# Kernel optimization log

Hardware: AMD Instinct MI355X
Metric: run time of the kernel (lower is better)

The kernel has to match this reference:

```python
import jax, jax.numpy as jnp
import numpy as np
import math

B, N, DIM, H, DH, NNULL = 2, 2048, 1024, 16, 64, 2
SCALE = 8.0
LN_EPS = 1e-5


def _alibi_slopes(heads):
    # heads is a power of 2 here (16): slopes = start * start**i
    start = 2.0 ** (-(2.0 ** (-(math.log2(heads) - 3))))
    return np.array([start * (start ** i) for i in range(heads)], dtype=np.float32)


def setup_inputs() -> dict:
    key = jax.random.key(0)
    ks = jax.random.split(key, 6)
    inner = H * DH
    return {
        "x": jax.random.normal(ks[0], (B, N, DIM), dtype=jnp.float32),
        "norm_g": jnp.ones((DIM,), jnp.float32),
        "norm_b": jnp.zeros((DIM,), jnp.float32),
        "Wq": jax.random.normal(ks[1], (DIM, inner), jnp.float32) * 0.02,
        "Wkv": jax.random.normal(ks[2], (DIM, 2 * inner), jnp.float32) * 0.02,
        "q_scale": jnp.ones((DH,), jnp.float32),
        "k_scale": jnp.ones((DH,), jnp.float32),
        "null_kv": jax.random.normal(ks[3], (H, 2 * NNULL, DH), jnp.float32),
        "Wout": jax.random.normal(ks[4], (inner, DIM), jnp.float32) * 0.02,
    }


def _l2norm(t):
    # matches F.normalize: x / max(||x||, 1e-12)
    n = jnp.sqrt(jnp.sum(t * t, axis=-1, keepdims=True))
    return t / jnp.maximum(n, 1e-12)


def reference(x, norm_g, norm_b, Wq, Wkv, q_scale, k_scale, null_kv, Wout):
    b, n, dim = x.shape
    h, dh, nn = H, DH, NNULL
    j = n + nn

    # NOTE: faithful to source -- K/V come from the PRE-norm x (kv_input bound
    # before x = self.norm(x)); only Q uses the LayerNorm'd x.
    mu = jnp.mean(x, axis=-1, keepdims=True)
    var = jnp.mean((x - mu) ** 2, axis=-1, keepdims=True)
    xn = (x - mu) * jax.lax.rsqrt(var + LN_EPS) * norm_g + norm_b

    q = (xn @ Wq).reshape(b, n, h, dh).transpose(0, 2, 1, 3)          # b h n d
    kv = x @ Wkv
    k, v = jnp.split(kv, 2, axis=-1)
    k = k.reshape(b, n, h, dh).transpose(0, 2, 1, 3)                   # b h n d
    v = v.reshape(b, n, h, dh).transpose(0, 2, 1, 3)

    # null kv: (h, 2*nn, dh) -> (h, nn, 2, dh)
    null = null_kv.reshape(h, nn, 2, dh)
    nk = jnp.broadcast_to(null[:, :, 0, :][None], (b, h, nn, dh))
    nv = jnp.broadcast_to(null[:, :, 1, :][None], (b, h, nn, dh))
    k = jnp.concatenate([nk, k], axis=2)                               # b h j d
    v = jnp.concatenate([nv, v], axis=2)

    q = _l2norm(q) * q_scale
    k = _l2norm(k) * k_scale

    sim = jnp.einsum('bhid,bhjd->bhij', q, k) * SCALE                  # b h n j

    # ALiBi bias: rows at positions j-n..j-1, cols 0..j-1
    irow = jnp.arange(j - n, j)
    jcol = jnp.arange(j)
    bias = -jnp.abs(jcol[None, :] - irow[:, None]).astype(sim.dtype)   # (n, j)
    slopes = jnp.asarray(_alibi_slopes(h))[:, None, None]              # (h,1,1)
    sim = sim + slopes * bias

    # causal mask: triu with offset j - n + 1 (null kv always visible)
    causal = jnp.triu(jnp.ones((n, j), dtype=bool), k=j - n + 1)
    neg = jnp.finfo(sim.dtype).max
    sim = jnp.where(causal[None, None], -neg, sim)

    attn = jax.nn.softmax(sim, axis=-1)
    out = jnp.einsum('bhij,bhjd->bhid', attn, v)
    out = out.transpose(0, 2, 1, 3).reshape(b, n, h * dh)
    return out @ Wout
```

## Files before the change

kernel.cpp:

```cpp
#include <hip/hip_runtime.h>
#include <hip/hip_bf16.h>
#include <stdint.h>

#define H_    16
#define N_    2048
#define DIM_  1024
#define DH_   64
#define NN_   2
#define J_    2050
#define JP_   2112
#define B_    2
#define M_    4096
#define NSEG_ 84

#define S8L_  11.541560327111707f
#define LOG2E_ 1.4426950408889634f

typedef unsigned short u16;
typedef unsigned int u32;
typedef short bf16x8 __attribute__((ext_vector_type(8)));
typedef float f32x4 __attribute__((ext_vector_type(4)));

__device__ __forceinline__ u16 f2b(float f) {
  union { float f; unsigned int i; } v; v.f = f;
  unsigned int r = v.i + 0x7fffu + ((v.i >> 16) & 1u);
  return (u16)(r >> 16);
}
__device__ __forceinline__ float b2f(u16 u) {
  union { unsigned int i; float f; } v; v.i = ((unsigned int)u) << 16; return v.f;
}
__device__ __forceinline__ float lo2f(u32 u) {
  union { u32 i; float f; } v; v.i = u << 16; return v.f;
}
__device__ __forceinline__ float hi2f(u32 u) {
  union { u32 i; float f; } v; v.i = u & 0xffff0000u; return v.f;
}
__device__ __forceinline__ void unp8(const uint4 u, float* d) {
  d[0] = lo2f(u.x); d[1] = hi2f(u.x); d[2] = lo2f(u.y); d[3] = hi2f(u.y);
  d[4] = lo2f(u.z); d[5] = hi2f(u.z); d[6] = lo2f(u.w); d[7] = hi2f(u.w);
}
__device__ __forceinline__ u32 pk2(float a, float b) {
  union { __hip_bfloat162 h; u32 u; } x;
  x.h = __float22bfloat162_rn(make_float2(a, b));
  return x.u;
}
__device__ __forceinline__ void dma16(const u16* g, u16* l) {
  __builtin_amdgcn_global_load_lds(
      (const __attribute__((address_space(1))) u32*)(const void*)g,
      (__attribute__((address_space(3))) u32*)(void*)l, 16, 0, 0);
}

__global__ __launch_bounds__(256) void ktranspose_cast(const float* __restrict__ in,
                                                       u16* __restrict__ out, int R, int C) {
  __shared__ float tile[32][33];
  int tx = threadIdx.x & 31, ty = threadIdx.x >> 5;
  int c0 = blockIdx.x * 32, r0 = blockIdx.y * 32;
  #pragma unroll
  for (int i = 0; i < 32; i += 8)
    tile[ty + i][tx] = in[(size_t)(r0 + ty + i) * C + c0 + tx];
  __syncthreads();
  #pragma unroll
  for (int i = 0; i < 32; i += 8)
    out[(size_t)(c0 + ty + i) * R + r0 + tx] = f2b(tile[tx][ty + i]);
}

__global__ __launch_bounds__(256) void lnorm_k(const float* __restrict__ x,
                                               const float* __restrict__ g,
                                               const float* __restrict__ bb,
                                               u16* __restrict__ xn,
                                               u16* __restrict__ xbf) {
  int row = blockIdx.x;
  int t = threadIdx.x;
  float4 rw = *(const float4*)(x + (size_t)row * DIM_ + t * 4);
  float v0 = rw.x, v1 = rw.y, v2 = rw.z, v3 = rw.w;
  uint2 cw;
  cw.x = pk2(v0, v1);
  cw.y = pk2(v2, v3);
  *(uint2*)(xbf + (size_t)row * DIM_ + t * 4) = cw;
  float s = v0 + v1 + v2 + v3;
  float ss = v0 * v0 + v1 * v1 + v2 * v2 + v3 * v3;
  #pragma unroll
  for (int o = 32; o; o >>= 1) { s += __shfl_xor(s, o, 64); ss += __shfl_xor(ss, o, 64); }
  __shared__ float red[8];
  int lane = t & 63, w = t >> 6;
  if (lane == 0) { red[w] = s; red[4 + w] = ss; }
  __syncthreads();
  float S = red[0] + red[1] + red[2] + red[3];
  float SS = red[4] + red[5] + red[6] + red[7];
  float mu = S * (1.0f / DIM_);
  float var = SS * (1.0f / DIM_) - mu * mu;
  float rs = rsqrtf(var + 1e-5f);
  float4 gv = *(const float4*)(g + t * 4);
  float4 bv = *(const float4*)(bb + t * 4);
  uint2 ow;
  ow.x = pk2((v0 - mu) * rs * gv.x + bv.x, (v1 - mu) * rs * gv.y + bv.y);
  ow.y = pk2((v2 - mu) * rs * gv.z + bv.z, (v3 - mu) * rs * gv.w + bv.w);
  *(uint2*)(xn + (size_t)row * DIM_ + t * 4) = ow;
}

template <int MODE>
__global__ __launch_bounds__(256) void gemm_k(const u16* __restrict__ A,
                                              const u16* __restrict__ BT,
                                              void* __restrict__ dst0,
                                              void* __restrict__ dst1,
                                              const float* __restrict__ scale,
                                              int M, int Nc, int K) {
  __shared__ u16 As[128 * 64];
  __shared__ u16 Bs[64 * 64];
  int tid = threadIdx.x, wv = tid >> 6, lane = tid & 63;
  int fm = lane & 15, fg = lane >> 4;
  int row0 = blockIdx.y * 128, col0 = blockIdx.x * 64;
  f32x4 acc[2][4] = {};
  int srow = lane >> 3;
  int skb = ((lane & 7) ^ srow) * 8;
  const u16* Ag = A + (size_t)(row0 + wv * 32 + srow) * K + skb;
  const u16* Bg = BT + (size_t)(col0 + wv * 16 + srow) * K + skb;
  u16* AsW = As + (wv * 32) * 64;
  u16* BsW = Bs + (wv * 16) * 64;
  int fr7 = fm & 7;
  int ak0 = (fg ^ fr7) * 8;
  int ak1 = ((fg + 4) ^ fr7) * 8;
  for (int k0 = 0; k0 < K; k0 += 64) {
    __syncthreads();
    dma16(Ag + k0,                    AsW);
    dma16(Ag + (size_t)8 * K + k0,    AsW + 8 * 64);
    dma16(Ag + (size_t)16 * K + k0,   AsW + 16 * 64);
    dma16(Ag + (size_t)24 * K + k0,   AsW + 24 * 64);
    dma16(Bg + k0,                    BsW);
    dma16(Bg + (size_t)8 * K + k0,    BsW + 8 * 64);
    __syncthreads();
    bf16x8 af0[2], af1[2], bf0[4], bf1[4];
    #pragma unroll
    for (int mt = 0; mt < 2; mt++) {
      int rbase = (wv * 32 + mt * 16 + fm) * 64;
      af0[mt] = *(const bf16x8*)&As[rbase + ak0];
      af1[mt] = *(const bf16x8*)&As[rbase + ak1];
    }
    #pragma unroll
    for (int nt = 0; nt < 4; nt++) {
      int rbase = (nt * 16 + fm) * 64;
      bf0[nt] = *(const bf16x8*)&Bs[rbase + ak0];
      bf1[nt] = *(const bf16x8*)&Bs[rbase + ak1];
    }
    #pragma unroll
    for (int mt = 0; mt < 2; mt++)
      #pragma unroll
      for (int nt = 0; nt < 4; nt++) {
        acc[mt][nt] = __builtin_amdgcn_mfma_f32_16x16x32_bf16(af0[mt], bf0[nt], acc[mt][nt], 0, 0, 0);
        acc[mt][nt] = __builtin_amdgcn_mfma_f32_16x16x32_bf16(af1[mt], bf1[nt], acc[mt][nt], 0, 0, 0);
      }
  }
  if (MODE == 1) {
    float* C = (float*)dst0;
    #pragma unroll
    for (int mt = 0; mt < 2; mt++)
      #pragma unroll
      for (int r = 0; r < 4; r++) {
        int m = row0 + wv * 32 + mt * 16 + fg * 4 + r;
        #pragma unroll
        for (int nt = 0; nt < 4; nt++)
          C[(size_t)m * Nc + col0 + nt * 16 + fm] = acc[mt][nt][r];
      }
  } else {
    bool isK = (MODE == 2) || (col0 < 1024);
    int h = (isK ? col0 : col0 - 1024) >> 6;
    float sv[4];
    if (isK) {
      #pragma unroll
      for (int nt = 0; nt < 4; nt++) sv[nt] = scale[nt * 16 + fm];
      if (MODE == 2) {
        #pragma unroll
        for (int nt = 0; nt < 4; nt++) sv[nt] *= S8L_;
      }
    }
    u16* Do = (u16*)((MODE == 3 && !isK) ? dst1 : dst0);
    #pragma unroll
    for (int mt = 0; mt < 2; mt++) {
      #pragma unroll
      for (int r = 0; r < 4; r++) {
        float inv = 1.0f;
        if (isK) {
          float ssp = 0.0f;
          #pragma unroll
          for (int nt = 0; nt < 4; nt++) ssp += acc[mt][nt][r] * acc[mt][nt][r];
          #pragma unroll
          for (int o = 1; o <= 8; o <<= 1) ssp += __shfl_xor(ssp, o, 64);
          inv = 1.0f / fmaxf(sqrtf(ssp), 1e-12f);
        }
        int m = row0 + wv * 32 + mt * 16 + fg * 4 + r;
        int b = m >> 11, n = m & 2047;
        size_t base;
        if (MODE == 2)      base = (((size_t)(b * H_ + h)) * N_ + n) * 64;
        else if (isK)       base = (((size_t)(b * H_ + h)) * JP_ + (n + NN_)) * 64;
        else                base = (((size_t)(b * H_ + h)) * J_ + (n + NN_)) * 64;
        #pragma unroll
        for (int nt = 0; nt < 4; nt++) {
          float val = acc[mt][nt][r];
          if (isK) val = val * inv * sv[nt];
          Do[base + nt * 16 + fm] = f2b(val);
        }
      }
    }
  }
}

__global__ __launch_bounds__(256) void vtransp_k(const u16* __restrict__ Vb,
                                                 const float* __restrict__ nkv,
                                                 const float* __restrict__ ks,
                                                 u16* __restrict__ Kb,
                                                 u16* __restrict__ VTp) {
  __shared__ u16 tile[64][80];
  int t = threadIdx.x;
  int c = blockIdx.x, bh = blockIdx.y, h = bh & 15;
  int jl = t >> 2, dc = (t & 3) * 16;
  int j = c * 64 + jl;
  if (j < NN_) {
    float kvv[16];
    float kssp = 0.0f;
    #pragma unroll
    for (int e = 0; e < 16; e++) {
      float vv = nkv[(size_t)(h * 4 + 2 * j + 1) * 64 + dc + e];
      tile[jl][dc + e] = f2b(vv);
      float kv = nkv[(size_t)(h * 4 + 2 * j) * 64 + dc + e];
      kvv[e] = kv; kssp += kv * kv;
    }
    kssp += __shfl_xor(kssp, 1, 64);
    kssp += __shfl_xor(kssp, 2, 64);
    float inv = 1.0f / fmaxf(sqrtf(kssp), 1e-12f);
    #pragma unroll
    for (int e = 0; e < 16; e++)
      Kb[((size_t)bh * JP_ + j) * 64 + dc + e] = f2b(kvv[e] * inv * ks[dc + e]);
  } else if (j < J_) {
    const uint4* src = (const uint4*)(Vb + ((size_t)bh * J_ + j) * 64 + dc);
    *(uint4*)&tile[jl][dc] = src[0];
    *(uint4*)&tile[jl][dc + 8] = src[1];
  } else {
    uint4 z = {0, 0, 0, 0};
    *(uint4*)&tile[jl][dc] = z;
    *(uint4*)&tile[jl][dc + 8] = z;
  }
  __syncthreads();
  int d = t >> 2, p0 = (t & 3) * 16;
  u16 tmp[16] __attribute__((aligned(16)));
  #pragma unroll
  for (int e = 0; e < 16; e++) {
    int pos = p0 + e;
    int h2 = pos >> 5, rem = pos & 31;
    int fgp = rem >> 3, tt = rem & 7;
    int nt = tt >> 2, r = tt & 3;
    int jloc = (h2 * 2 + nt) * 16 + fgp * 4 + r;
    tmp[e] = tile[jloc][d];
  }
  uint4* dstp = (uint4*)(VTp + ((size_t)bh * 64 + d) * JP_ + c * 64 + p0);
  dstp[0] = ((uint4*)tmp)[0];
  dstp[1] = ((uint4*)tmp)[1];
}

__global__ __launch_bounds__(256, 6) void attn_k(const u16* __restrict__ Qn,
                                                 const u16* __restrict__ Kb,
                                                 const u16* __restrict__ VTp,
                                                 const float* __restrict__ qs,
                                                 const float* __restrict__ ks,
                                                 u16* __restrict__ partials) {
  __shared__ u16 Ks0[64 * 32], Ks1[64 * 32];
  __shared__ u16 Vs0[64 * 32], Vs1[64 * 32];
  int tid = threadIdx.x;
  int wv = tid >> 6, lane = tid & 63;
  int fm = lane & 15, fg = lane >> 4;
  int bh = blockIdx.y, h = bh & 15;
  int cum = 0, qt = 0, seg = 0;
  #pragma unroll 1
  for (int i = 0; i < 32; i++) {
    int t = 31 - i, s = (t + 9) >> 3;
    if ((int)blockIdx.x < cum + s) { qt = t; seg = (int)blockIdx.x - cum; break; }
    cum += s;
  }
  int q0 = qt * 64;
  int q = q0 + wv * 16 + fm;
  float slope = exp2f(-0.5f * (float)(h + 1));
  float prod = fabsf(qs[lane] * ks[lane]);
  #pragma unroll
  for (int o = 32; o; o >>= 1) prod = fmaxf(prod, __shfl_xor(prod, o, 64));
  float MbL = 8.0f * prod * LOG2E_;
  float slopeL = slope * LOG2E_;
  const u16* qp = Qn + ((size_t)bh * N_ + q) * 64 + fg * 8;
  bf16x8 qf0 = *(const bf16x8*)(qp);
  bf16x8 qf1 = *(const bf16x8*)(qp + 32);
  f32x4 accO[4] = {};
  float lp = 0.0f;
  int lr = lane >> 2;
  int kbs = ((lane & 3) ^ ((lane >> 3) & 3)) * 8;
  int fs = (fg ^ ((fm >> 1) & 3)) * 8;
  const u16* KbBH = Kb + (size_t)bh * JP_ * 64;
  const u16* VTbh = VTp + (size_t)bh * 64 * JP_;
  int c0 = seg * 8;
  int c1 = min(c0 + 8, qt + 2);
  float bias0 = slopeL * (float)(c0 * 64 + fg * 4 - q - 2) - MbL;
  float sr1 = slopeL, sr2 = slopeL * 2.0f, sr3 = slopeL * 3.0f;
  float s16 = slopeL * 16.0f;
  float d64 = slopeL * 64.0f;
  for (int c = c0; c < c1; c++) {
    int jb = c * 64;
    __syncthreads();
    const u16* Kg = KbBH + (size_t)(jb + wv * 16 + lr) * 64 + kbs;
    dma16(Kg,      Ks0 + wv * 512);
    dma16(Kg + 32, Ks1 + wv * 512);
    const u16* Vg = VTbh + (size_t)(wv * 16 + lr) * JP_ + jb + kbs;
    dma16(Vg,      Vs0 + wv * 512);
    dma16(Vg + 32, Vs1 + wv * 512);
    __syncthreads();
    f32x4 accS[4] = {};
    #pragma unroll
    for (int nt = 0; nt < 4; nt++) {
      bf16x8 kf0 = *(const bf16x8*)&Ks0[(nt * 16 + fm) * 32 + fs];
      accS[nt] = __builtin_amdgcn_mfma_f32_16x16x32_bf16(kf0, qf0, accS[nt], 0, 0, 0);
      bf16x8 kf1 = *(const bf16x8*)&Ks1[(nt * 16 + fm) * 32 + fs];
      accS[nt] = __builtin_amdgcn_mfma_f32_16x16x32_bf16(kf1, qf1, accS[nt], 0, 0, 0);
    }
    union { bf16x8 v; u32 u[4]; } P0, P1;
    float lps = 0.0f;
    float bnt = bias0;
    if (c < qt) {
      #pragma unroll
      for (int nt = 0; nt < 4; nt++) {
        float e0 = __builtin_amdgcn_exp2f(accS[nt][0] + bnt);
        float e1 = __builtin_amdgcn_exp2f((accS[nt][1] + sr1) + bnt);
        float e2 = __builtin_amdgcn_exp2f((accS[nt][2] + sr2) + bnt);
        float e3 = __builtin_amdgcn_exp2f((accS[nt][3] + sr3) + bnt);
        u32 w0 = pk2(e0, e1);
        u32 w1 = pk2(e2, e3);
        lps += (e0 + e1) + (e2 + e3);
        if (nt < 2) { P0.u[nt * 2] = w0; P0.u[nt * 2 + 1] = w1; }
        else        { P1.u[(nt - 2) * 2] = w0; P1.u[(nt - 2) * 2 + 1] = w1; }
        bnt += s16;
      }
    } else {
      int thr = q + 2 - jb;
      #pragma unroll
      for (int nt = 0; nt < 4; nt++) {
        int ib = nt * 16 + fg * 4;
        float e0 = __builtin_amdgcn_exp2f(accS[nt][0] + bnt);
        float e1 = __builtin_amdgcn_exp2f((accS[nt][1] + sr1) + bnt);
        float e2 = __builtin_amdgcn_exp2f((accS[nt][2] + sr2) + bnt);
        float e3 = __builtin_amdgcn_exp2f((accS[nt][3] + sr3) + bnt);
        e0 = (ib + 0 <= thr) ? e0 : 0.0f;
        e1 = (ib + 1 <= thr) ? e1 : 0.0f;
        e2 = (ib + 2 <= thr) ? e2 : 0.0f;
        e3 = (ib + 3 <= thr) ? e3 : 0.0f;
        u32 w0 = pk2(e0, e1);
        u32 w1 = pk2(e2, e3);
        lps += (e0 + e1) + (e2 + e3);
        if (nt < 2) { P0.u[nt * 2] = w0; P0.u[nt * 2 + 1] = w1; }
        else        { P1.u[(nt - 2) * 2] = w0; P1.u[(nt - 2) * 2 + 1] = w1; }
        bnt += s16;
      }
    }
    lp += lps;
    bias0 += d64;
    #pragma unroll
    for (int nt = 0; nt < 4; nt++) {
      bf16x8 vf0 = *(const bf16x8*)&Vs0[(nt * 16 + fm) * 32 + fs];
      accO[nt] = __builtin_amdgcn_mfma_f32_16x16x32_bf16(vf0, P0.v, accO[nt], 0, 0, 0);
      bf16x8 vf1 = *(const bf16x8*)&Vs1[(nt * 16 + fm) * 32 + fs];
      accO[nt] = __builtin_amdgcn_mfma_f32_16x16x32_bf16(vf1, P1.v, accO[nt], 0, 0, 0);
    }
  }
  lp += __shfl_xor(lp, 16, 64);
  lp += __shfl_xor(lp, 32, 64);
  u16* P = partials + ((size_t)bh * NSEG_ + blockIdx.x) * 4224;
  int sq = wv * 16 + fm;
  #pragma unroll
  for (int nt = 0; nt < 4; nt++) {
    uint2 ow;
    ow.x = pk2(accO[nt][0], accO[nt][1]);
    ow.y = pk2(accO[nt][2], accO[nt][3]);
    *(uint2*)(P + sq * 64 + nt * 16 + fg * 4) = ow;
  }
  if (fg == 0) *(float*)(P + 4096 + 2 * sq) = lp;
}

__global__ __launch_bounds__(256) void comb_k(const u16* __restrict__ partials,
                                              u16* __restrict__ AO) {
  int qt = blockIdx.x, bh = blockIdx.y, b = bh >> 4, h = bh & 15;
  int t = threadIdx.x, q = t >> 2, dq = (t & 3) * 16;
  int s = (qt + 9) >> 3;
  int cum = 0;
  for (int tt = qt + 1; tt < 32; tt++) cum += (tt + 9) >> 3;
  float acc[16] = {};
  float lsum = 0.0f;
  for (int k = 0; k < s; k++) {
    const u16* P = partials + ((size_t)bh * NSEG_ + cum + k) * 4224;
    uint4 a = *(const uint4*)(P + q * 64 + dq);
    uint4 bq = *(const uint4*)(P + q * 64 + dq + 8);
    float tmp[8];
    unp8(a, tmp);
    #pragma unroll
    for (int e = 0; e < 8; e++) acc[e] += tmp[e];
    unp8(bq, tmp);
    #pragma unroll
    for (int e = 0; e < 8; e++) acc[8 + e] += tmp[e];
    lsum += *(const float*)(P + 4096 + 2 * q);
  }
  float linv = 1.0f / lsum;
  int n = qt * 64 + q;
  u16* dst = AO + (((size_t)(b * N_ + n)) * H_ + h) * 64 + dq;
  u16 ov[16] __attribute__((aligned(16)));
  #pragma unroll
  for (int e = 0; e < 16; e++) ov[e] = f2b(acc[e] * linv);
  *(uint4*)dst = ((uint4*)ov)[0];
  *(uint4*)(dst + 8) = ((uint4*)ov)[1];
}

extern "C" void kernel_launch(void* const* d_in, const int* in_sizes, int n_in,
                              void* d_out, int out_size, void* d_ws, size_t ws_size,
                              hipStream_t stream) {
  const float* x    = (const float*)d_in[0];
  const float* ng   = (const float*)d_in[1];
  const float* nb   = (const float*)d_in[2];
  const float* Wq   = (const float*)d_in[3];
  const float* Wkv  = (const float*)d_in[4];
  const float* qs   = (const float*)d_in[5];
  const float* ks   = (const float*)d_in[6];
  const float* nkv  = (const float*)d_in[7];
  const float* Wout = (const float*)d_in[8];
  float* out = (float*)d_out;
  char* ws = (char*)d_ws;

  u16* xn    = (u16*)(ws + 0);
  u16* WoutT = (u16*)(ws + 8388608);
  u16* Qn    = (u16*)(ws + 10485760);
  u16* Kb    = (u16*)(ws + 18874368);
  u16* VTp   = (u16*)(ws + 27525120);
  u16* xbf   = (u16*)(ws + 36175872);
  u16* WqT   = (u16*)(ws + 44564480);
  u16* WkvT  = (u16*)(ws + 46661632);
  u16* Vb    = (u16*)(ws + 50855936);
  u16* parts = xbf;
  u16* AO    = xn;

  hipMemsetAsync(Kb, 0, 8650752, stream);
  ktranspose_cast<<<dim3(32, 32), 256, 0, stream>>>(Wq, WqT, 1024, 1024);
  ktranspose_cast<<<dim3(64, 32), 256, 0, stream>>>(Wkv, WkvT, 1024, 2048);
  ktranspose_cast<<<dim3(32, 32), 256, 0, stream>>>(Wout, WoutT, 1024, 1024);
  lnorm_k<<<4096, 256, 0, stream>>>(x, ng, nb, xn, xbf);
  gemm_k<2><<<dim3(16, 32), 256, 0, stream>>>(xn, WqT, Qn, nullptr, qs, M_, 1024, 1024);
  gemm_k<3><<<dim3(32, 32), 256, 0, stream>>>(xbf, WkvT, Kb, Vb, ks, M_, 2048, 1024);
  vtransp_k<<<dim3(33, 32), 256, 0, stream>>>(Vb, nkv, ks, Kb, VTp);
  attn_k<<<dim3(NSEG_, 32), 256, 0, stream>>>(Qn, Kb, VTp, qs, ks, parts);
  comb_k<<<dim3(32, 32), 256, 0, stream>>>(parts, AO);
  gemm_k<1><<<dim3(16, 32), 256, 0, stream>>>(AO, WoutT, out, nullptr, nullptr, M_, 1024, 1024);
}
```

Baseline: 218.4 us.

## Double-buffer K/V shared tiles in attention kernel to overlap loads with MFMA

```diff
diff --git a/kernel.cpp b/kernel.cpp
--- a/kernel.cpp
+++ b/kernel.cpp
@@ -256,14 +256,14 @@
   dstp[1] = ((uint4*)tmp)[1];
 }
 
-__global__ __launch_bounds__(256, 6) void attn_k(const u16* __restrict__ Qn,
+__global__ __launch_bounds__(256, 5) void attn_k(const u16* __restrict__ Qn,
                                                  const u16* __restrict__ Kb,
                                                  const u16* __restrict__ VTp,
                                                  const float* __restrict__ qs,
                                                  const float* __restrict__ ks,
                                                  u16* __restrict__ partials) {
-  __shared__ u16 Ks0[64 * 32], Ks1[64 * 32];
-  __shared__ u16 Vs0[64 * 32], Vs1[64 * 32];
+  __shared__ u16 Ks0[2][64 * 32], Ks1[2][64 * 32];
+  __shared__ u16 Vs0[2][64 * 32], Vs1[2][64 * 32];
   int tid = threadIdx.x;
   int wv = tid >> 6, lane = tid & 63;
   int fm = lane & 15, fg = lane >> 4;
@@ -299,22 +299,33 @@
   float sr1 = slopeL, sr2 = slopeL * 2.0f, sr3 = slopeL * 3.0f;
   float s16 = slopeL * 16.0f;
   float d64 = slopeL * 64.0f;
+  {
+    int jb = c0 * 64;
+    const u16* Kg = KbBH + (size_t)(jb + wv * 16 + lr) * 64 + kbs;
+    dma16(Kg,      Ks0[0] + wv * 512);
+    dma16(Kg + 32, Ks1[0] + wv * 512);
+    const u16* Vg = VTbh + (size_t)(wv * 16 + lr) * JP_ + jb + kbs;
+    dma16(Vg,      Vs0[0] + wv * 512);
+    dma16(Vg + 32, Vs1[0] + wv * 512);
+  }
+  __syncthreads();
+  int cur = 0;
   for (int c = c0; c < c1; c++) {
-    int jb = c * 64;
-    __syncthreads();
-    const u16* Kg = KbBH + (size_t)(jb + wv * 16 + lr) * 64 + kbs;
-    dma16(Kg,      Ks0 + wv * 512);
-    dma16(Kg + 32, Ks1 + wv * 512);
-    const u16* Vg = VTbh + (size_t)(wv * 16 + lr) * JP_ + jb + kbs;
-    dma16(Vg,      Vs0 + wv * 512);
-    dma16(Vg + 32, Vs1 + wv * 512);
-    __syncthreads();
+    if (c + 1 < c1) {
+      int jb = (c + 1) * 64;
+      const u16* Kg = KbBH + (size_t)(jb + wv * 16 + lr) * 64 + kbs;
+      dma16(Kg,      Ks0[cur ^ 1] + wv * 512);
+      dma16(Kg + 32, Ks1[cur ^ 1] + wv * 512);
+      const u16* Vg = VTbh + (size_t)(wv * 16 + lr) * JP_ + jb + kbs;
+      dma16(Vg,      Vs0[cur ^ 1] + wv * 512);
+      dma16(Vg + 32, Vs1[cur ^ 1] + wv * 512);
+    }
     f32x4 accS[4] = {};
     #pragma unroll
     for (int nt = 0; nt < 4; nt++) {
-      bf16x8 kf0 = *(const bf16x8*)&Ks0[(nt * 16 + fm) * 32 + fs];
+      bf16x8 kf0 = *(const bf16x8*)&Ks0[cur][(nt * 16 + fm) * 32 + fs];
       accS[nt] = __builtin_amdgcn_mfma_f32_16x16x32_bf16(kf0, qf0, accS[nt], 0, 0, 0);
-      bf16x8 kf1 = *(const bf16x8*)&Ks1[(nt * 16 + fm) * 32 + fs];
+      bf16x8 kf1 = *(const bf16x8*)&Ks1[cur][(nt * 16 + fm) * 32 + fs];
       accS[nt] = __builtin_amdgcn_mfma_f32_16x16x32_bf16(kf1, qf1, accS[nt], 0, 0, 0);
     }
     union { bf16x8 v; u32 u[4]; } P0, P1;
@@ -335,6 +346,7 @@
         bnt += s16;
       }
     } else {
+      int jb = c * 64;
       int thr = q + 2 - jb;
       #pragma unroll
       for (int nt = 0; nt < 4; nt++) {
@@ -359,11 +371,13 @@
     bias0 += d64;
     #pragma unroll
     for (int nt = 0; nt < 4; nt++) {
-      bf16x8 vf0 = *(const bf16x8*)&Vs0[(nt * 16 + fm) * 32 + fs];
+      bf16x8 vf0 = *(const bf16x8*)&Vs0[cur][(nt * 16 + fm) * 32 + fs];
       accO[nt] = __builtin_amdgcn_mfma_f32_16x16x32_bf16(vf0, P0.v, accO[nt], 0, 0, 0);
-      bf16x8 vf1 = *(const bf16x8*)&Vs1[(nt * 16 + fm) * 32 + fs];
+      bf16x8 vf1 = *(const bf16x8*)&Vs1[cur][(nt * 16 + fm) * 32 + fs];
       accO[nt] = __builtin_amdgcn_mfma_f32_16x16x32_bf16(vf1, P1.v, accO[nt], 0, 0, 0);
     }
+    __syncthreads();
+    cur ^= 1;
   }
   lp += __shfl_xor(lp, 16, 64);
   lp += __shfl_xor(lp, 32, 64);
```

New measurement: 222.1 us. About the same (+1.7%).
